# Performance work log

Hardware: AMD Instinct MI355X
Metric: run time of the kernel (lower is better)

The kernel has to match this reference:

```python
import jax, jax.numpy as jnp
import numpy as np

N_NODES = 50000
N_EDGES = 800000
IN_CH, HID, LAT = 256, 128, 64


def setup_inputs() -> dict:
    key = jax.random.key(0)
    k1, k2, k3, k4 = jax.random.split(key, 4)
    x = jax.random.normal(k1, (N_NODES, IN_CH), dtype=jnp.float32)
    edge_index = jax.random.randint(k2, (2, N_EDGES), 0, N_NODES, dtype=jnp.int64)
    W1 = jax.random.normal(k3, (IN_CH, HID), dtype=jnp.float32) * (1.0 / np.sqrt(IN_CH))
    b1 = jnp.zeros((HID,), dtype=jnp.float32)
    W2 = jax.random.normal(k4, (HID, LAT), dtype=jnp.float32) * (1.0 / np.sqrt(HID))
    b2 = jnp.zeros((LAT,), dtype=jnp.float32)
    return {"x": x, "edge_index": edge_index, "W1": W1, "b1": b1, "W2": W2, "b2": b2}


def gcn_conv(x, src, dst, deg_inv_sqrt, W, b):
    # PyG GCNConv: h = x @ W; out[dst] += d_dst^-1/2 * d_src^-1/2 * h[src]; + bias
    h = x @ W                                   # [N, out]
    norm = deg_inv_sqrt[src] * deg_inv_sqrt[dst]  # [E+N]
    msg = h[src] * norm[:, None]                # [E+N, out] (gather + scale)
    out = jax.ops.segment_sum(msg, dst, num_segments=x.shape[0])
    return out + b


def reference(x, edge_index, W1, b1, W2, b2):
    n = x.shape[0]
    loop = jnp.arange(n, dtype=edge_index.dtype)
    # add self loops (GCNConv default)
    src = jnp.concatenate([edge_index[0], loop])
    dst = jnp.concatenate([edge_index[1], loop])
    deg = jax.ops.segment_sum(jnp.ones_like(dst, dtype=x.dtype), dst, num_segments=n)
    deg_inv_sqrt = jnp.where(deg > 0, jax.lax.rsqrt(deg), 0.0)
    h = jax.nn.relu(gcn_conv(x, src, dst, deg_inv_sqrt, W1, b1))
    h = jax.nn.relu(gcn_conv(h, src, dst, deg_inv_sqrt, W2, b2))
    return h
```

## Files before the change

### kernel.cpp

```cpp
#include <hip/hip_runtime.h>

#define N_NODES 50000
#define N_EDGES 800000
#define IN_CH 256
#define HID 128
#define LAT 64
#define CAP 64
#define NBIN 196
#define BINCAP 4864

typedef __attribute__((ext_vector_type(8))) short short8;
typedef __attribute__((ext_vector_type(16))) float f32x16;

static __device__ __forceinline__ unsigned short bf16_rne(float x) {
    unsigned u = __float_as_uint(x);
    unsigned r = (u + 0x7FFFu + ((u >> 16) & 1u)) >> 16;
    return (unsigned short)r;
}
static __device__ __forceinline__ float bf16_to_f(unsigned short h) {
    return __uint_as_float(((unsigned)h) << 16);
}

static __device__ __forceinline__ void add8(uint4 p, float* a) {
    a[0] += __uint_as_float(p.x << 16);
    a[1] += __uint_as_float(p.x & 0xFFFF0000u);
    a[2] += __uint_as_float(p.y << 16);
    a[3] += __uint_as_float(p.y & 0xFFFF0000u);
    a[4] += __uint_as_float(p.z << 16);
    a[5] += __uint_as_float(p.z & 0xFFFF0000u);
    a[6] += __uint_as_float(p.w << 16);
    a[7] += __uint_as_float(p.w & 0xFFFF0000u);
}
static __device__ __forceinline__ void fma8(uint4 p, float m, float* a) {
    a[0] = fmaf(m, __uint_as_float(p.x << 16), a[0]);
    a[1] = fmaf(m, __uint_as_float(p.x & 0xFFFF0000u), a[1]);
    a[2] = fmaf(m, __uint_as_float(p.y << 16), a[2]);
    a[3] = fmaf(m, __uint_as_float(p.y & 0xFFFF0000u), a[3]);
    a[4] = fmaf(m, __uint_as_float(p.z << 16), a[4]);
    a[5] = fmaf(m, __uint_as_float(p.z & 0xFFFF0000u), a[5]);
    a[6] = fmaf(m, __uint_as_float(p.w << 16), a[6]);
    a[7] = fmaf(m, __uint_as_float(p.w & 0xFFFF0000u), a[7]);
}

template <int K, int NN>
static __device__ __forceinline__ void split_store(const float* __restrict__ W,
                                                   unsigned short* __restrict__ Wf, int i) {
    constexpr int CT = NN / 32;
    int k = i / NN, n = i % NN;
    float w = W[i];
    unsigned short hi = bf16_rne(w);
    unsigned short lo = bf16_rne(w - bf16_to_f(hi));
    size_t off = ((size_t)((k >> 4) * CT + (n >> 5)) * 64 + ((n & 31) + 32 * ((k >> 3) & 1))) * 8 + (k & 7);
    Wf[off] = hi;
    Wf[(size_t)K * NN + off] = lo;
}

__global__ __launch_bounds__(256) void prep_kernel(const float* __restrict__ W1,
                                                   const float* __restrict__ W2,
                                                   int* __restrict__ binCnt,
                                                   unsigned short* __restrict__ W1f,
                                                   unsigned short* __restrict__ W2f) {
    int i = blockIdx.x * blockDim.x + threadIdx.x;
    if (i < NBIN) binCnt[i] = 0;
    if (i < IN_CH * HID) split_store<IN_CH, HID>(W1, W1f, i);
    if (i < HID * LAT) split_store<HID, LAT>(W2, W2f, i);
}

__global__ __launch_bounds__(256) void fill1_kernel(const int* __restrict__ ei,
                                                    int* __restrict__ binCnt,
                                                    unsigned int* __restrict__ binBuf, int E) {
    __shared__ int hist[NBIN];
    __shared__ int base[NBIN];
    const int tid = threadIdx.x;
    for (int i = tid; i < NBIN; i += 256) hist[i] = 0;
    __syncthreads();

    const int e0 = blockIdx.x * 2048 + tid;
    unsigned int pk[8];
    int bn[8], ofs[8];
#pragma unroll
    for (int i = 0; i < 8; ++i) {
        int e = e0 + 256 * i;
        bool v = e < E;
        int s = v ? ei[e] : 0;
        int d = v ? ei[E + e] : 0;
        bn[i] = d >> 8;
        pk[i] = (unsigned int)s | ((unsigned int)(d & 255) << 16);
        ofs[i] = v ? atomicAdd(&hist[bn[i]], 1) : -1;
    }
    __syncthreads();
    for (int i = tid; i < NBIN; i += 256)
        base[i] = hist[i] ? atomicAdd(&binCnt[i], hist[i]) : 0;
    __syncthreads();
#pragma unroll
    for (int i = 0; i < 8; ++i) {
        if (ofs[i] >= 0) {
            int p = base[bn[i]] + ofs[i];
            if (p < BINCAP) binBuf[(size_t)bn[i] * BINCAP + p] = pk[i];
        }
    }
}

__global__ __launch_bounds__(256) void fill2_kernel(const int* __restrict__ binCnt,
                                                    const unsigned int* __restrict__ binBuf,
                                                    int* __restrict__ cnt,
                                                    unsigned short* __restrict__ colb) {
    __shared__ int lcnt[256];
    const int b = blockIdx.x;
    const int tid = threadIdx.x;
    lcnt[tid] = 0;
    __syncthreads();
    int n = binCnt[b]; if (n > BINCAP) n = BINCAP;
    const int node0 = b << 8;
    for (int i = tid; i < n; i += 256) {
        unsigned int pk = binBuf[(size_t)b * BINCAP + i];
        int local = pk >> 16;
        int s = pk & 0xFFFF;
        int slot = atomicAdd(&lcnt[local], 1);
        if (slot < CAP) colb[(size_t)(node0 + local) * CAP + slot] = (unsigned short)s;
    }
    __syncthreads();
    int node = node0 + tid;
    if (node < N_NODES) cnt[node] = lcnt[tid];
}

template <int K, int NN>
__global__ __launch_bounds__(256) void gemm_kernel(const float* __restrict__ A,
                                                   const unsigned short* __restrict__ Wf,
                                                   const int* __restrict__ cnt,
                                                   unsigned short* __restrict__ C, int M) {
    constexpr int CT = NN / 32;
    constexpr int MT = (NN == 128) ? 2 : 1;
    __shared__ unsigned short As[16 * 512];
    __shared__ unsigned short Bs[2 * 2 * CT * 512];

    const int tid = threadIdx.x;
    const int lane = tid & 63;
    const int w = tid >> 6;
    const int row0 = blockIdx.x * 128;
    const int rtb = (NN == 128) ? ((w >> 1) * 2) : w;
    const int ctb = (NN == 128) ? ((w & 1) * 2) : 0;

    f32x16 acc[MT][2];
#pragma unroll
    for (int mt = 0; mt < MT; ++mt)
#pragma unroll
        for (int nt = 0; nt < 2; ++nt)
#pragma unroll
            for (int q = 0; q < 16; ++q) acc[mt][nt][q] = 0.0f;

    for (int kt = 0; kt < K; kt += 32) {
#pragma unroll
        for (int i = 0; i < 4; ++i) {
            int f = tid + 256 * i;
            int m = f >> 3, kq = f & 7;
            int row = row0 + m; if (row >= M) row = M - 1;
            const float4 v = *(const float4*)(A + (size_t)row * K + kt + kq * 4);
            ushort4 hi4 = make_ushort4(bf16_rne(v.x), bf16_rne(v.y), bf16_rne(v.z), bf16_rne(v.w));
            ushort4 lo4 = make_ushort4(bf16_rne(v.x - bf16_to_f(hi4.x)),
                                       bf16_rne(v.y - bf16_to_f(hi4.y)),
                                       bf16_rne(v.z - bf16_to_f(hi4.z)),
                                       bf16_rne(v.w - bf16_to_f(hi4.w)));
            int k0 = kq * 4;
            int s = k0 >> 4, half = (k0 >> 3) & 1, j0 = k0 & 7, t = m >> 5;
            int ln = (m & 31) + 32 * half;
            *(ushort4*)&As[(((s) * 4 + t) << 9) + (ln << 3) + j0] = hi4;
            *(ushort4*)&As[((((2 + s)) * 4 + t) << 9) + (ln << 3) + j0] = lo4;
        }
        {
            const int sg0 = kt >> 4;
#pragma unroll
            for (int p = 0; p < 2; ++p)
#pragma unroll
                for (int sl = 0; sl < 2; ++sl) {
                    const float4* src = (const float4*)(Wf + (size_t)p * K * NN + (size_t)(sg0 + sl) * CT * 512);
                    float4* dst = (float4*)(Bs + (((p * 2 + sl) * CT) << 9));
                    for (int i = tid; i < CT * 64; i += 256) dst[i] = src[i];
                }
        }
        __syncthreads();

#pragma unroll
        for (int sl = 0; sl < 2; ++sl) {
            short8 ah[MT], al[MT], bh[2], bl[2];
#pragma unroll
            for (int mt = 0; mt < MT; ++mt) {
                ah[mt] = *(const short8*)&As[((sl * 4 + rtb + mt) << 9) + (lane << 3)];
                al[mt] = *(const short8*)&As[(((2 + sl) * 4 + rtb + mt) << 9) + (lane << 3)];
            }
#pragma unroll
            for (int nt = 0; nt < 2; ++nt) {
                bh[nt] = *(const short8*)&Bs[((sl * CT + ctb + nt) << 9) + (lane << 3)];
                bl[nt] = *(const short8*)&Bs[(((2 + sl) * CT + ctb + nt) << 9) + (lane << 3)];
            }
#pragma unroll
            for (int mt = 0; mt < MT; ++mt)
#pragma unroll
                for (int nt = 0; nt < 2; ++nt) {
                    acc[mt][nt] = __builtin_amdgcn_mfma_f32_32x32x16_bf16(ah[mt], bh[nt], acc[mt][nt], 0, 0, 0);
                    acc[mt][nt] = __builtin_amdgcn_mfma_f32_32x32x16_bf16(ah[mt], bl[nt], acc[mt][nt], 0, 0, 0);
                    acc[mt][nt] = __builtin_amdgcn_mfma_f32_32x32x16_bf16(al[mt], bh[nt], acc[mt][nt], 0, 0, 0);
                }
        }
        __syncthreads();
    }

#pragma unroll
    for (int mt = 0; mt < MT; ++mt) {
#pragma unroll
        for (int r = 0; r < 16; ++r) {
            int rowl = (rtb + mt) * 32 + (r & 3) + 8 * (r >> 2) + 4 * (lane >> 5);
            int row = row0 + rowl;
            if (row < M) {
                float sc = rsqrtf((float)cnt[row] + 1.0f);
#pragma unroll
                for (int nt = 0; nt < 2; ++nt) {
                    int col = (ctb + nt) * 32 + (lane & 31);
                    C[(size_t)row * NN + col] = bf16_rne(acc[mt][nt][r] * sc);
                }
            }
        }
    }
}

template <int C>
__global__ __launch_bounds__(256) void agg_kernel(const int* __restrict__ cnt,
                                                  const unsigned short* __restrict__ colb,
                                                  const unsigned short* __restrict__ hs,
                                                  const float* __restrict__ bias,
                                                  float* __restrict__ out, int N) {
    constexpr int LPN = C / 8;
    constexpr int NPW = 64 / LPN;
    int node = (int)((blockIdx.x * blockDim.x + threadIdx.x) >> 6);
    int lane = threadIdx.x & 63;
    if (node >= N) return;
    const int g = lane / LPN;
    const int c = lane % LPN;

    int deg = cnt[node];
    int kk = deg < CAP ? deg : CAP;

    float acc[8];
#pragma unroll
    for (int q = 0; q < 8; ++q) acc[q] = 0.0f;
    if (g == 0) add8(*(const uint4*)(hs + (size_t)node * C + c * 8), acc);

    int myc = (lane < kk) ? (int)colb[(size_t)node * CAP + lane] : 0;

    int j = 0;
    for (; j + NPW * 4 <= kk; j += NPW * 4) {
        int s0 = __shfl(myc, j + g);
        int s1 = __shfl(myc, j + g + NPW);
        int s2 = __shfl(myc, j + g + 2 * NPW);
        int s3 = __shfl(myc, j + g + 3 * NPW);
        uint4 p0 = *(const uint4*)(hs + (size_t)s0 * C + c * 8);
        uint4 p1 = *(const uint4*)(hs + (size_t)s1 * C + c * 8);
        uint4 p2 = *(const uint4*)(hs + (size_t)s2 * C + c * 8);
        uint4 p3 = *(const uint4*)(hs + (size_t)s3 * C + c * 8);
        add8(p0, acc); add8(p1, acc); add8(p2, acc); add8(p3, acc);
    }
    if (j < kk) {
        bool v0 = (j + g) < kk, v1 = (j + g + NPW) < kk,
             v2 = (j + g + 2 * NPW) < kk, v3 = (j + g + 3 * NPW) < kk;
        int s0 = __shfl(myc, v0 ? (j + g) : 0);
        int s1 = __shfl(myc, v1 ? (j + g + NPW) : 0);
        int s2 = __shfl(myc, v2 ? (j + g + 2 * NPW) : 0);
        int s3 = __shfl(myc, v3 ? (j + g + 3 * NPW) : 0);
        uint4 p0 = *(const uint4*)(hs + (size_t)s0 * C + c * 8);
        uint4 p1 = *(const uint4*)(hs + (size_t)s1 * C + c * 8);
        uint4 p2 = *(const uint4*)(hs + (size_t)s2 * C + c * 8);
        uint4 p3 = *(const uint4*)(hs + (size_t)s3 * C + c * 8);
        fma8(p0, v0 ? 1.0f : 0.0f, acc);
        fma8(p1, v1 ? 1.0f : 0.0f, acc);
        fma8(p2, v2 ? 1.0f : 0.0f, acc);
        fma8(p3, v3 ? 1.0f : 0.0f, acc);
    }

#pragma unroll
    for (int s = LPN; s < 64; s <<= 1)
#pragma unroll
        for (int q = 0; q < 8; ++q) acc[q] += __shfl_xor(acc[q], s);

    if (lane < LPN) {
        float di = rsqrtf((float)deg + 1.0f);
        const float4 b0 = *(const float4*)(bias + c * 8);
        const float4 b1 = *(const float4*)(bias + c * 8 + 4);
        float4 o0, o1;
        o0.x = fmaxf(fmaf(di, acc[0], b0.x), 0.0f);
        o0.y = fmaxf(fmaf(di, acc[1], b0.y), 0.0f);
        o0.z = fmaxf(fmaf(di, acc[2], b0.z), 0.0f);
        o0.w = fmaxf(fmaf(di, acc[3], b0.w), 0.0f);
        o1.x = fmaxf(fmaf(di, acc[4], b1.x), 0.0f);
        o1.y = fmaxf(fmaf(di, acc[5], b1.y), 0.0f);
        o1.z = fmaxf(fmaf(di, acc[6], b1.z), 0.0f);
        o1.w = fmaxf(fmaf(di, acc[7], b1.w), 0.0f);
        *(float4*)(out + (size_t)node * C + c * 8) = o0;
        *(float4*)(out + (size_t)node * C + c * 8 + 4) = o1;
    }
}

extern "C" void kernel_launch(void* const* d_in, const int* in_sizes, int n_in,
                              void* d_out, int out_size, void* d_ws, size_t ws_size,
                              hipStream_t stream) {
    const float* x  = (const float*)d_in[0];
    const int*   ei = (const int*)d_in[1];
    const float* W1 = (const float*)d_in[2];
    const float* b1 = (const float*)d_in[3];
    const float* W2 = (const float*)d_in[4];
    const float* b2 = (const float*)d_in[5];
    float* out = (float*)d_out;

    const int N = N_NODES, E = N_EDGES;

    char* ws = (char*)d_ws;
    size_t off = 0;
    auto alloc = [&](size_t bytes) {
        void* p = ws + off;
        off = (off + bytes + 255) & ~(size_t)255;
        return p;
    };
    int*            cnt    = (int*)alloc((size_t)N * 4);
    unsigned short* colb   = (unsigned short*)alloc((size_t)N * CAP * 2);
    int*            binCnt = (int*)alloc((size_t)NBIN * 4);
    unsigned int*   binBuf = (unsigned int*)alloc((size_t)NBIN * BINCAP * 4);
    unsigned short* W1f    = (unsigned short*)alloc((size_t)2 * IN_CH * HID * 2);
    unsigned short* W2f    = (unsigned short*)alloc((size_t)2 * HID * LAT * 2);
    unsigned short* h1s    = (unsigned short*)alloc((size_t)N * HID * 2);
    float*          act1   = (float*)alloc((size_t)N * HID * 4);
    unsigned short* h2s    = h1s;

    prep_kernel<<<(N + 255) / 256, 256, 0, stream>>>(W1, W2, binCnt, W1f, W2f);
    fill1_kernel<<<(E + 2047) / 2048, 256, 0, stream>>>(ei, binCnt, binBuf, E);
    fill2_kernel<<<NBIN, 256, 0, stream>>>(binCnt, binBuf, cnt, colb);

    gemm_kernel<IN_CH, HID><<<(N + 127) / 128, 256, 0, stream>>>(x, W1f, cnt, h1s, N);
    agg_kernel<HID><<<(N + 3) / 4, 256, 0, stream>>>(cnt, colb, h1s, b1, act1, N);

    gemm_kernel<HID, LAT><<<(N + 127) / 128, 256, 0, stream>>>(act1, W2f, cnt, h2s, N);
    agg_kernel<LAT><<<(N + 3) / 4, 256, 0, stream>>>(cnt, colb, h2s, b2, out, N);
}
```

Baseline: 209.5 us.

## Drop activation lo-split in GEMMs, store layer-1 activations as bf16, use LDS direct loads

The GEMM now converts the A operand to a single bf16 value instead of a hi/lo pair, which cuts the MFMA count from three to two per tile and halves A's shared-memory footprint. The first aggregation writes its ReLU output as bf16, so the intermediate activation tensor is half the size and the second GEMM loads bf16 directly with no conversion. Weight tiles are copied into LDS with global_load_lds instead of going through registers. The trade is lower accuracy on the activations (weights keep their hi/lo split), which may put the result near the tolerance.

```diff
diff --git a/kernel.cpp b/kernel.cpp
--- a/kernel.cpp
+++ b/kernel.cpp
@@ -124,14 +124,14 @@
     if (node < N_NODES) cnt[node] = lcnt[tid];
 }
 
-template <int K, int NN>
-__global__ __launch_bounds__(256) void gemm_kernel(const float* __restrict__ A,
+template <int K, int NN, bool AFP32>
+__global__ __launch_bounds__(256) void gemm_kernel(const void* __restrict__ Av,
                                                    const unsigned short* __restrict__ Wf,
                                                    const int* __restrict__ cnt,
                                                    unsigned short* __restrict__ C, int M) {
     constexpr int CT = NN / 32;
     constexpr int MT = (NN == 128) ? 2 : 1;
-    __shared__ unsigned short As[16 * 512];
+    __shared__ unsigned short As[8 * 512];
     __shared__ unsigned short Bs[2 * 2 * CT * 512];
 
     const int tid = threadIdx.x;
@@ -150,22 +150,32 @@
             for (int q = 0; q < 16; ++q) acc[mt][nt][q] = 0.0f;
 
     for (int kt = 0; kt < K; kt += 32) {
-#pragma unroll
-        for (int i = 0; i < 4; ++i) {
-            int f = tid + 256 * i;
-            int m = f >> 3, kq = f & 7;
-            int row = row0 + m; if (row >= M) row = M - 1;
-            const float4 v = *(const float4*)(A + (size_t)row * K + kt + kq * 4);
-            ushort4 hi4 = make_ushort4(bf16_rne(v.x), bf16_rne(v.y), bf16_rne(v.z), bf16_rne(v.w));
-            ushort4 lo4 = make_ushort4(bf16_rne(v.x - bf16_to_f(hi4.x)),
-                                       bf16_rne(v.y - bf16_to_f(hi4.y)),
-                                       bf16_rne(v.z - bf16_to_f(hi4.z)),
-                                       bf16_rne(v.w - bf16_to_f(hi4.w)));
-            int k0 = kq * 4;
-            int s = k0 >> 4, half = (k0 >> 3) & 1, j0 = k0 & 7, t = m >> 5;
-            int ln = (m & 31) + 32 * half;
-            *(ushort4*)&As[(((s) * 4 + t) << 9) + (ln << 3) + j0] = hi4;
-            *(ushort4*)&As[((((2 + s)) * 4 + t) << 9) + (ln << 3) + j0] = lo4;
+        if constexpr (AFP32) {
+            const float* A = (const float*)Av;
+#pragma unroll
+            for (int i = 0; i < 4; ++i) {
+                int f = tid + 256 * i;
+                int m = f >> 3, kq = f & 7;
+                int row = row0 + m; if (row >= M) row = M - 1;
+                const float4 v = *(const float4*)(A + (size_t)row * K + kt + kq * 4);
+                ushort4 hi4 = make_ushort4(bf16_rne(v.x), bf16_rne(v.y), bf16_rne(v.z), bf16_rne(v.w));
+                int k0 = kq * 4;
+                int s = k0 >> 4, half = (k0 >> 3) & 1, j0 = k0 & 7, t = m >> 5;
+                int ln = (m & 31) + 32 * half;
+                *(ushort4*)&As[((s * 4 + t) << 9) + (ln << 3) + j0] = hi4;
+            }
+        } else {
+            const unsigned short* A = (const unsigned short*)Av;
+#pragma unroll
+            for (int i = 0; i < 2; ++i) {
+                int f = tid + 256 * i;
+                int m = f >> 2, kc = f & 3;
+                int row = row0 + m; if (row >= M) row = M - 1;
+                uint4 v = *(const uint4*)(A + (size_t)row * K + kt + kc * 8);
+                int s = kc >> 1, half = kc & 1, t = m >> 5;
+                int ln = (m & 31) + 32 * half;
+                *(uint4*)&As[((s * 4 + t) << 9) + (ln << 3)] = v;
+            }
         }
         {
             const int sg0 = kt >> 4;
@@ -175,19 +185,22 @@
                 for (int sl = 0; sl < 2; ++sl) {
                     const float4* src = (const float4*)(Wf + (size_t)p * K * NN + (size_t)(sg0 + sl) * CT * 512);
                     float4* dst = (float4*)(Bs + (((p * 2 + sl) * CT) << 9));
-                    for (int i = tid; i < CT * 64; i += 256) dst[i] = src[i];
+                    for (int c0 = w * 64; c0 < CT * 64; c0 += 256) {
+                        __builtin_amdgcn_global_load_lds(
+                            (const __attribute__((address_space(1))) unsigned int*)(src + c0 + lane),
+                            (__attribute__((address_space(3))) unsigned int*)(dst + c0),
+                            16, 0, 0);
+                    }
                 }
         }
         __syncthreads();
 
 #pragma unroll
         for (int sl = 0; sl < 2; ++sl) {
-            short8 ah[MT], al[MT], bh[2], bl[2];
-#pragma unroll
-            for (int mt = 0; mt < MT; ++mt) {
-                ah[mt] = *(const short8*)&As[((sl * 4 + rtb + mt) << 9) + (lane << 3)];
-                al[mt] = *(const short8*)&As[(((2 + sl) * 4 + rtb + mt) << 9) + (lane << 3)];
-            }
+            short8 a[MT], bh[2], bl[2];
+#pragma unroll
+            for (int mt = 0; mt < MT; ++mt)
+                a[mt] = *(const short8*)&As[((sl * 4 + rtb + mt) << 9) + (lane << 3)];
 #pragma unroll
             for (int nt = 0; nt < 2; ++nt) {
                 bh[nt] = *(const short8*)&Bs[((sl * CT + ctb + nt) << 9) + (lane << 3)];
@@ -197,9 +210,8 @@
             for (int mt = 0; mt < MT; ++mt)
 #pragma unroll
                 for (int nt = 0; nt < 2; ++nt) {
-                    acc[mt][nt] = __builtin_amdgcn_mfma_f32_32x32x16_bf16(ah[mt], bh[nt], acc[mt][nt], 0, 0, 0);
-                    acc[mt][nt] = __builtin_amdgcn_mfma_f32_32x32x16_bf16(ah[mt], bl[nt], acc[mt][nt], 0, 0, 0);
-                    acc[mt][nt] = __builtin_amdgcn_mfma_f32_32x32x16_bf16(al[mt], bh[nt], acc[mt][nt], 0, 0, 0);
+                    acc[mt][nt] = __builtin_amdgcn_mfma_f32_32x32x16_bf16(a[mt], bh[nt], acc[mt][nt], 0, 0, 0);
+                    acc[mt][nt] = __builtin_amdgcn_mfma_f32_32x32x16_bf16(a[mt], bl[nt], acc[mt][nt], 0, 0, 0);
                 }
         }
         __syncthreads();
@@ -223,12 +235,12 @@
     }
 }
 
-template <int C>
+template <int C, bool OBF16>
 __global__ __launch_bounds__(256) void agg_kernel(const int* __restrict__ cnt,
                                                   const unsigned short* __restrict__ colb,
                                                   const unsigned short* __restrict__ hs,
                                                   const float* __restrict__ bias,
-                                                  float* __restrict__ out, int N) {
+                                                  void* __restrict__ outv, int N) {
     constexpr int LPN = C / 8;
     constexpr int NPW = 64 / LPN;
     int node = (int)((blockIdx.x * blockDim.x + threadIdx.x) >> 6);
@@ -283,19 +295,23 @@
 
     if (lane < LPN) {
         float di = rsqrtf((float)deg + 1.0f);
-        const float4 b0 = *(const float4*)(bias + c * 8);
-        const float4 b1 = *(const float4*)(bias + c * 8 + 4);
-        float4 o0, o1;
-        o0.x = fmaxf(fmaf(di, acc[0], b0.x), 0.0f);
-        o0.y = fmaxf(fmaf(di, acc[1], b0.y), 0.0f);
-        o0.z = fmaxf(fmaf(di, acc[2], b0.z), 0.0f);
-        o0.w = fmaxf(fmaf(di, acc[3], b0.w), 0.0f);
-        o1.x = fmaxf(fmaf(di, acc[4], b1.x), 0.0f);
-        o1.y = fmaxf(fmaf(di, acc[5], b1.y), 0.0f);
-        o1.z = fmaxf(fmaf(di, acc[6], b1.z), 0.0f);
-        o1.w = fmaxf(fmaf(di, acc[7], b1.w), 0.0f);
-        *(float4*)(out + (size_t)node * C + c * 8) = o0;
-        *(float4*)(out + (size_t)node * C + c * 8 + 4) = o1;
+        float o[8];
+#pragma unroll
+        for (int q = 0; q < 8; ++q)
+            o[q] = fmaxf(fmaf(di, acc[q], bias[c * 8 + q]), 0.0f);
+        if constexpr (OBF16) {
+            unsigned short* out = (unsigned short*)outv;
+            ushort4 lo4 = make_ushort4(bf16_rne(o[0]), bf16_rne(o[1]), bf16_rne(o[2]), bf16_rne(o[3]));
+            ushort4 hi4 = make_ushort4(bf16_rne(o[4]), bf16_rne(o[5]), bf16_rne(o[6]), bf16_rne(o[7]));
+            *(ushort4*)(out + (size_t)node * C + c * 8) = lo4;
+            *(ushort4*)(out + (size_t)node * C + c * 8 + 4) = hi4;
+        } else {
+            float* out = (float*)outv;
+            float4 o0 = {o[0], o[1], o[2], o[3]};
+            float4 o1 = {o[4], o[5], o[6], o[7]};
+            *(float4*)(out + (size_t)node * C + c * 8) = o0;
+            *(float4*)(out + (size_t)node * C + c * 8 + 4) = o1;
+        }
     }
 }
 
@@ -308,7 +324,6 @@
     const float* b1 = (const float*)d_in[3];
     const float* W2 = (const float*)d_in[4];
     const float* b2 = (const float*)d_in[5];
-    float* out = (float*)d_out;
 
     const int N = N_NODES, E = N_EDGES;
 
@@ -326,16 +341,16 @@
     unsigned short* W1f    = (unsigned short*)alloc((size_t)2 * IN_CH * HID * 2);
     unsigned short* W2f    = (unsigned short*)alloc((size_t)2 * HID * LAT * 2);
     unsigned short* h1s    = (unsigned short*)alloc((size_t)N * HID * 2);
-    float*          act1   = (float*)alloc((size_t)N * HID * 4);
+    unsigned short* act1   = (unsigned short*)alloc((size_t)N * HID * 2);
     unsigned short* h2s    = h1s;
 
     prep_kernel<<<(N + 255) / 256, 256, 0, stream>>>(W1, W2, binCnt, W1f, W2f);
     fill1_kernel<<<(E + 2047) / 2048, 256, 0, stream>>>(ei, binCnt, binBuf, E);
     fill2_kernel<<<NBIN, 256, 0, stream>>>(binCnt, binBuf, cnt, colb);
 
-    gemm_kernel<IN_CH, HID><<<(N + 127) / 128, 256, 0, stream>>>(x, W1f, cnt, h1s, N);
-    agg_kernel<HID><<<(N + 3) / 4, 256, 0, stream>>>(cnt, colb, h1s, b1, act1, N);
-
-    gemm_kernel<HID, LAT><<<(N + 127) / 128, 256, 0, stream>>>(act1, W2f, cnt, h2s, N);
-    agg_kernel<LAT><<<(N + 3) / 4, 256, 0, stream>>>(cnt, colb, h2s, b2, out, N);
-}
+    gemm_kernel<IN_CH, HID, true><<<(N + 127) / 128, 256, 0, stream>>>(x, W1f, cnt, h1s, N);
+    agg_kernel<HID, true><<<(N + 3) / 4, 256, 0, stream>>>(cnt, colb, h1s, b1, act1, N);
+
+    gemm_kernel<HID, LAT, false><<<(N + 127) / 128, 256, 0, stream>>>(act1, W2f, cnt, h2s, N);
+    agg_kernel<LAT, false><<<(N + 3) / 4, 256, 0, stream>>>(cnt, colb, h2s, b2, d_out, N);
+}
```

Result: no change. 213.6 us (+2.0%).
